# Kernel tuning notes

Measured on AMD Instinct MI355X. Metric: run time of the kernel, lower is better.

Reference implementation:

```python
import jax, jax.numpy as jnp
import numpy as np

DIM, D_STATE, D_CONV, EXPAND = 384, 16, 4, 2
D_INNER = EXPAND * DIM          # 768
DT_RANK = -(-DIM // 16)         # 24
B_, T_, H_, W_ = 2, 8, 16, 16
EPS = 1e-5


def layernorm(x, w, b):
    mu = x.mean(-1, keepdims=True)
    var = ((x - mu) ** 2).mean(-1, keepdims=True)
    return (x - mu) * jax.lax.rsqrt(var + EPS) * w + b


def setup_inputs() -> dict:
    key = jax.random.key(0)
    ks = jax.random.split(key, 12)
    std = 0.02
    x = jax.random.normal(ks[0], (B_, DIM, T_, H_, W_), jnp.float32)
    params = dict(
        ln1_w=jnp.ones((DIM,), jnp.float32),
        ln1_b=jnp.zeros((DIM,), jnp.float32),
        ln2_w=jnp.ones((DIM,), jnp.float32),
        ln2_b=jnp.zeros((DIM,), jnp.float32),
        in_proj_w=std * jax.random.normal(ks[1], (2 * D_INNER, DIM), jnp.float32),
        conv_w=std * jax.random.normal(ks[2], (D_INNER, 1, D_CONV), jnp.float32),
        conv_b=jnp.zeros((D_INNER,), jnp.float32),
        x_proj_w=std * jax.random.normal(ks[3], (DT_RANK + 2 * D_STATE, D_INNER), jnp.float32),
        dt_proj_w=std * jax.random.normal(ks[4], (D_INNER, DT_RANK), jnp.float32),
        dt_proj_b=0.01 * jax.random.normal(ks[5], (D_INNER,), jnp.float32),
        A_log=jnp.log(jnp.broadcast_to(jnp.arange(1, D_STATE + 1, dtype=jnp.float32), (D_INNER, D_STATE))),
        D=jnp.ones((D_INNER,), jnp.float32),
        out_proj_w=std * jax.random.normal(ks[6], (DIM, D_INNER), jnp.float32),
    )
    return {"x": x, **params}


def mamba(xn, in_proj_w, conv_w, conv_b, x_proj_w, dt_proj_w, dt_proj_b, A_log, D, out_proj_w):
    # xn: [B, L, dim]
    B, L, _ = xn.shape
    xz = xn @ in_proj_w.T                      # [B, L, 2*d_inner]
    u, z = jnp.split(xz, 2, axis=-1)
    # causal depthwise conv over tokens
    uc = jnp.transpose(u, (0, 2, 1))           # [B, d_inner, L]
    uc = jax.lax.conv_general_dilated(
        uc, conv_w, window_strides=(1,), padding=[(D_CONV - 1, 0)],
        dimension_numbers=("NCH", "OIH", "NCH"), feature_group_count=D_INNER)
    u = jax.nn.silu(jnp.transpose(uc, (0, 2, 1)) + conv_b)  # [B, L, d_inner]

    dbc = u @ x_proj_w.T                       # [B, L, dt_rank + 2*d_state]
    dt = dbc[..., :DT_RANK]
    Bm = dbc[..., DT_RANK:DT_RANK + D_STATE]   # [B, L, d_state]
    Cm = dbc[..., DT_RANK + D_STATE:]          # [B, L, d_state]
    delta = jax.nn.softplus(dt @ dt_proj_w.T + dt_proj_b)   # [B, L, d_inner]

    A = -jnp.exp(A_log)                        # [d_inner, d_state]
    deltaA = jnp.exp(delta[..., None] * A)                     # [B, L, d_inner, d_state]
    deltaBu = delta[..., None] * Bm[:, :, None, :] * u[..., None]

    def step(h, inp):
        dA, dBu, c = inp                       # [B,d_inner,d_state], [B,d_inner,d_state], [B,d_state]
        h = dA * h + dBu
        y = jnp.einsum("bds,bs->bd", h, c)
        return h, y

    h0 = jnp.zeros((B, D_INNER, D_STATE), xn.dtype)
    xs = (jnp.moveaxis(deltaA, 1, 0), jnp.moveaxis(deltaBu, 1, 0), jnp.moveaxis(Cm, 1, 0))
    _, ys = jax.lax.scan(step, h0, xs)
    y = jnp.moveaxis(ys, 0, 1)                 # [B, L, d_inner]
    y = y + u * D
    y = y * jax.nn.silu(z)
    return y @ out_proj_w.T                    # [B, L, dim]


def reference(x, ln1_w, ln1_b, ln2_w, ln2_b, in_proj_w, conv_w, conv_b,
              x_proj_w, dt_proj_w, dt_proj_b, A_log, D, out_proj_w):
    B, C, T, H, W = x.shape
    L = T * H * W
    x_flat = jnp.transpose(x.reshape(B, C, L), (0, 2, 1))   # [B, L, C]
    x_norm = layernorm(x_flat, ln1_w, ln1_b)
    x_mamba = mamba(x_norm, in_proj_w, conv_w, conv_b, x_proj_w,
                    dt_proj_w, dt_proj_b, A_log, D, out_proj_w)
    x_out = layernorm(x_flat + x_mamba, ln2_w, ln2_b)
    return jnp.transpose(x_out, (0, 2, 1)).reshape(B, C, T, H, W)
```

## Files before the change

kernel.cpp:

```cpp
#include <hip/hip_runtime.h>
#include <hip/hip_bf16.h>

typedef unsigned short u16;
typedef unsigned int   u32;
typedef __attribute__((ext_vector_type(8))) short short8;
typedef __attribute__((ext_vector_type(4))) float f32x4;

#define B_   2
#define L_   2048
#define CDIM 384
#define DI   768
#define DXZ  1536
#define DTR  24
#define DS   16
#define NDBC 56
#define NC   64
#define TC   32
#define TL   32
#define EPSV 1e-5f

#define OFFW_WIN  0
#define OFFW_WXP  589824
#define OFFW_WOUT 632832
#define TOTW      927744

__device__ __forceinline__ float bf2f(u16 u) {
    union { u32 i; float f; } v; v.i = ((u32)u) << 16; return v.f;
}
__device__ __forceinline__ u16 f2bf(float f) {
    union { float f; u32 i; } v; v.f = f;
    u32 x = v.i;
    u32 r = (x + 0x7FFFu + ((x >> 16) & 1u)) >> 16;
    return (u16)r;
}

__global__ __launch_bounds__(256) void ln1_convert(const float* __restrict__ x,
                                                   const float* __restrict__ w,
                                                   const float* __restrict__ bb,
                                                   u16* __restrict__ xn,
                                                   const float* __restrict__ win,
                                                   const float* __restrict__ wxp,
                                                   const float* __restrict__ wout,
                                                   u16* __restrict__ wdst) {
    __shared__ float tile[CDIM][TL + 1];
    __shared__ float red_s[8][TL];
    __shared__ float red_s2[8][TL];
    __shared__ float mu_s[TL], rs_s[TL];
    int tid = threadIdx.x, blk = blockIdx.x;
    if (blk >= 128) {
        int base = (blk - 128) * 256 + tid;
        for (int e = base; e < TOTW; e += 128 * 256) {
            float v;
            if (e < OFFW_WXP)       v = win[e];
            else if (e < OFFW_WOUT) v = wxp[e - OFFW_WXP];
            else                    v = wout[e - OFFW_WOUT];
            wdst[e] = f2bf(v);
        }
        return;
    }
    int b = blk >> 6;
    int l0 = (blk & 63) * TL;
    int cg = tid >> 5, li = tid & 31;
    const float* xp = x + (size_t)b * CDIM * L_ + l0 + li;
    float s = 0.f, s2 = 0.f;
#pragma unroll
    for (int c = cg; c < CDIM; c += 8) {
        float v = xp[(size_t)c * L_];
        tile[c][li] = v;
        s += v; s2 += v * v;
    }
    red_s[cg][li] = s; red_s2[cg][li] = s2;
    __syncthreads();
    if (tid < TL) {
        float ts = 0.f, ts2 = 0.f;
#pragma unroll
        for (int g = 0; g < 8; g++) { ts += red_s[g][tid]; ts2 += red_s2[g][tid]; }
        float mu = ts / CDIM;
        float var = ts2 / CDIM - mu * mu;
        mu_s[tid] = mu; rs_s[tid] = rsqrtf(var + EPSV);
    }
    __syncthreads();
    int wv = tid >> 6, lane = tid & 63;
#pragma unroll
    for (int r = 0; r < 8; r++) {
        int l = wv * 8 + r;
        float mu = mu_s[l], rs = rs_s[l];
        u16* op = xn + (size_t)(b * L_ + l0 + l) * CDIM;
#pragma unroll
        for (int j = 0; j < 6; j++) {
            int c = lane + 64 * j;
            float t = (tile[c][l] - mu) * rs * w[c] + bb[c];
            op[c] = f2bf(t);
        }
    }
}

template<int KN>
__global__ __launch_bounds__(256) void gemm_in(const u16* __restrict__ A,
                                               const u16* __restrict__ Bm,
                                               u16* __restrict__ Cp, int Nn) {
    int wave = threadIdx.x >> 6, lane = threadIdx.x & 63;
    int wm = wave & 1, wn = wave >> 1;
    int m0 = (blockIdx.x * 2 + wm) * 64;
    int n0 = (blockIdx.y * 2 + wn) * 64;
    int r = lane & 15, q = lane >> 4;
    f32x4 acc[4][4];
#pragma unroll
    for (int i = 0; i < 4; i++)
#pragma unroll
        for (int j = 0; j < 4; j++)
#pragma unroll
            for (int g = 0; g < 4; g++) acc[i][j][g] = 0.f;
#pragma unroll
    for (int k0 = 0; k0 < KN; k0 += 32) {
        short8 af[4], bf[4];
        int ka = k0 + q * 8;
#pragma unroll
        for (int i = 0; i < 4; i++) {
            af[i] = *(const short8*)(A + (size_t)(m0 + i * 16 + r) * KN + ka);
            bf[i] = *(const short8*)(Bm + (size_t)(n0 + i * 16 + r) * KN + ka);
        }
#pragma unroll
        for (int i = 0; i < 4; i++)
#pragma unroll
            for (int j = 0; j < 4; j++)
                acc[i][j] = __builtin_amdgcn_mfma_f32_16x16x32_bf16(af[i], bf[j], acc[i][j], 0, 0, 0);
    }
#pragma unroll
    for (int i = 0; i < 4; i++)
#pragma unroll
        for (int j = 0; j < 4; j++) {
            int col = n0 + j * 16 + r;
#pragma unroll
            for (int g = 0; g < 4; g++)
                Cp[(size_t)(m0 + i * 16 + q * 4 + g) * Nn + col] = f2bf(acc[i][j][g]);
        }
}

template<int KN, int NN>
__global__ __launch_bounds__(64) void gemm_out(const u16* __restrict__ A,
                                               const u16* __restrict__ Bm,
                                               float* __restrict__ Cp) {
    int lane = threadIdx.x;
    int m0 = blockIdx.x * 64, n0 = blockIdx.y * 64;
    int r = lane & 15, q = lane >> 4;
    f32x4 acc[4][4];
#pragma unroll
    for (int i = 0; i < 4; i++)
#pragma unroll
        for (int j = 0; j < 4; j++)
#pragma unroll
            for (int g = 0; g < 4; g++) acc[i][j][g] = 0.f;
#pragma unroll
    for (int k0 = 0; k0 < KN; k0 += 32) {
        short8 af[4], bf[4];
        int ka = k0 + q * 8;
#pragma unroll
        for (int i = 0; i < 4; i++) {
            af[i] = *(const short8*)(A + (size_t)(m0 + i * 16 + r) * KN + ka);
            bf[i] = *(const short8*)(Bm + (size_t)(n0 + i * 16 + r) * KN + ka);
        }
#pragma unroll
        for (int i = 0; i < 4; i++)
#pragma unroll
            for (int j = 0; j < 4; j++)
                acc[i][j] = __builtin_amdgcn_mfma_f32_16x16x32_bf16(af[i], bf[j], acc[i][j], 0, 0, 0);
    }
#pragma unroll
    for (int i = 0; i < 4; i++)
#pragma unroll
        for (int j = 0; j < 4; j++) {
            int col = n0 + j * 16 + r;
#pragma unroll
            for (int g = 0; g < 4; g++)
                Cp[(size_t)(m0 + i * 16 + q * 4 + g) * NN + col] = acc[i][j][g];
        }
}

template<int KN>
__global__ __launch_bounds__(64) void gemm_xp(const u16* __restrict__ A,
                                              const u16* __restrict__ Bm,
                                              float* __restrict__ Cp) {
    int lane = threadIdx.x;
    int m0 = blockIdx.x * 16;
    int r = lane & 15, q = lane >> 4;
    f32x4 acc[4];
#pragma unroll
    for (int j = 0; j < 4; j++)
#pragma unroll
        for (int g = 0; g < 4; g++) acc[j][g] = 0.f;
    short8 zf;
#pragma unroll
    for (int e = 0; e < 8; e++) zf[e] = 0;
#pragma unroll
    for (int k0 = 0; k0 < KN; k0 += 32) {
        int ka = k0 + q * 8;
        short8 af = *(const short8*)(A + (size_t)(m0 + r) * KN + ka);
        short8 bf[4];
#pragma unroll
        for (int j = 0; j < 4; j++) {
            int n = j * 16 + r;
            bf[j] = (n < NDBC) ? *(const short8*)(Bm + (size_t)n * KN + ka) : zf;
        }
#pragma unroll
        for (int j = 0; j < 4; j++)
            acc[j] = __builtin_amdgcn_mfma_f32_16x16x32_bf16(af, bf[j], acc[j], 0, 0, 0);
    }
#pragma unroll
    for (int j = 0; j < 4; j++) {
        int col = j * 16 + r;
        if (col < NDBC) {
#pragma unroll
            for (int g = 0; g < 4; g++)
                Cp[(size_t)(m0 + q * 4 + g) * NDBC + col] = acc[j][g];
        }
    }
}

__global__ __launch_bounds__(256) void conv_silu(const u16* __restrict__ xz,
                                                 const float* __restrict__ cw,
                                                 const float* __restrict__ cb,
                                                 u16* __restrict__ ubf) {
    int d = blockIdx.y * 256 + threadIdx.x;
    int m0 = blockIdx.x * 16;
    int l0 = m0 & (L_ - 1);
    float4 c4 = ((const float4*)cw)[d];
    float bias = cb[d];
    float w0, w1, w2;
    if (l0 == 0) { w0 = w1 = w2 = 0.f; }
    else {
        w0 = bf2f(xz[(size_t)(m0 - 3) * DXZ + d]);
        w1 = bf2f(xz[(size_t)(m0 - 2) * DXZ + d]);
        w2 = bf2f(xz[(size_t)(m0 - 1) * DXZ + d]);
    }
#pragma unroll
    for (int i = 0; i < 16; i++) {
        int m = m0 + i;
        float cur = bf2f(xz[(size_t)m * DXZ + d]);
        float acc = bias + w0 * c4.x + w1 * c4.y + w2 * c4.z + cur * c4.w;
        float sg = 1.f / (1.f + __expf(-acc));
        ubf[(size_t)m * DI + d] = f2bf(acc * sg);
        w0 = w1; w1 = w2; w2 = cur;
    }
}

__global__ __launch_bounds__(256) void scan_pass1(const u16* __restrict__ ubf,
                                                  const float* __restrict__ dbc,
                                                  const float* __restrict__ alogf,
                                                  const float* __restrict__ wdtf,
                                                  const float* __restrict__ bdtf,
                                                  float* __restrict__ chA,
                                                  float* __restrict__ chB) {
    int bc = blockIdx.x;
    int b = bc >> 6, chunk = bc & 63;
    int d = blockIdx.y * 256 + threadIdx.x;
    float a[DS], ap[DS], bv[DS], wdt[DTR];
#pragma unroll
    for (int s = 0; s < DS; s++) { a[s] = -__expf(alogf[d * DS + s]); ap[s] = 1.f; bv[s] = 0.f; }
#pragma unroll
    for (int k = 0; k < DTR; k++) wdt[k] = wdtf[d * DTR + k];
    float bd = bdtf[d];
    int t0 = b * L_ + chunk * TC;
#pragma unroll 2
    for (int t = t0; t < t0 + TC; t++) {
        const float* row = dbc + (size_t)t * NDBC;
        float acc = bd;
#pragma unroll
        for (int k = 0; k < DTR; k++) acc += row[k] * wdt[k];
        float dd = (acc > 20.f) ? acc : __logf(1.f + __expf(acc));
        float du = dd * bf2f(ubf[(size_t)t * DI + d]);
#pragma unroll
        for (int s = 0; s < DS; s++) {
            float dA = __expf(dd * a[s]);
            bv[s] = dA * bv[s] + du * row[DTR + s];
            ap[s] *= dA;
        }
    }
    float* pa = chA + ((size_t)bc * DI + d) * DS;
    float* pb = chB + ((size_t)bc * DI + d) * DS;
#pragma unroll
    for (int s = 0; s < DS; s++) { pa[s] = ap[s]; pb[s] = bv[s]; }
}

__global__ __launch_bounds__(256) void scan_mid(const float* __restrict__ chA,
                                                const float* __restrict__ chB,
                                                float* __restrict__ hin) {
    int idx = blockIdx.x * 256 + threadIdx.x;
    int b = idx / (DI * DS);
    int rem = idx - b * (DI * DS);
    float h = 0.f;
#pragma unroll 4
    for (int c = 0; c < NC; c++) {
        size_t off = ((size_t)(b * NC + c) * DI) * DS + rem;
        hin[off] = h;
        h = chA[off] * h + chB[off];
    }
}

__global__ __launch_bounds__(256) void scan_pass2(const u16* __restrict__ ubf,
                                                  const float* __restrict__ dbc,
                                                  const float* __restrict__ alogf,
                                                  const float* __restrict__ wdtf,
                                                  const float* __restrict__ bdtf,
                                                  const float* __restrict__ hin,
                                                  const float* __restrict__ Dwf,
                                                  const u16* __restrict__ xz,
                                                  u16* __restrict__ ym) {
    int bc = blockIdx.x;
    int b = bc >> 6, chunk = bc & 63;
    int d = blockIdx.y * 256 + threadIdx.x;
    float a[DS], h[DS], wdt[DTR];
#pragma unroll
    for (int s = 0; s < DS; s++) a[s] = -__expf(alogf[d * DS + s]);
#pragma unroll
    for (int k = 0; k < DTR; k++) wdt[k] = wdtf[d * DTR + k];
    float bd = bdtf[d];
    const float* hp = hin + ((size_t)bc * DI + d) * DS;
    float h0[DS];
#pragma unroll
    for (int s = 0; s < DS; s++) h[s] = hp[s];
    float dD = Dwf[d];
    int t0 = b * L_ + chunk * TC;
#pragma unroll 2
    for (int t = t0; t < t0 + TC; t++) {
        const float* row = dbc + (size_t)t * NDBC;
        float acc = bd;
#pragma unroll
        for (int k = 0; k < DTR; k++) acc += row[k] * wdt[k];
        float dd = (acc > 20.f) ? acc : __logf(1.f + __expf(acc));
        float uu = bf2f(ubf[(size_t)t * DI + d]);
        float du = dd * uu;
        float y = 0.f;
#pragma unroll
        for (int s = 0; s < DS; s++) {
            float dA = __expf(dd * a[s]);
            h[s] = dA * h[s] + du * row[DTR + s];
            y += h[s] * row[DTR + DS + s];
        }
        float z = bf2f(xz[(size_t)t * DXZ + DI + d]);
        float sg = 1.f / (1.f + __expf(-z));
        ym[(size_t)t * DI + d] = f2bf((y + uu * dD) * (z * sg));
    }
}

__global__ __launch_bounds__(256) void ln2_out(const float* __restrict__ x,
                                               const float* __restrict__ om,
                                               const float* __restrict__ w,
                                               const float* __restrict__ bb,
                                               float* __restrict__ out) {
    __shared__ float tile[CDIM][TL + 1];
    __shared__ float mu_s[TL], rs_s[TL];
    int tid = threadIdx.x, blk = blockIdx.x;
    int b = blk >> 6;
    int l0 = (blk & 63) * TL;
    int cg = tid >> 5, li = tid & 31;
    const float* xp = x + (size_t)b * CDIM * L_ + l0 + li;
#pragma unroll
    for (int c = cg; c < CDIM; c += 8) tile[c][li] = xp[(size_t)c * L_];
    __syncthreads();
    int wv = tid >> 6, lane = tid & 63;
#pragma unroll
    for (int r = 0; r < 8; r++) {
        int l = wv * 8 + r;
        const float* op = om + (size_t)(b * L_ + l0 + l) * CDIM;
        float s = 0.f, s2 = 0.f;
#pragma unroll
        for (int j = 0; j < 6; j++) {
            int c = lane + 64 * j;
            float t = tile[c][l] + op[c];
            tile[c][l] = t;
            s += t; s2 += t * t;
        }
#pragma unroll
        for (int off = 32; off > 0; off >>= 1) { s += __shfl_xor(s, off); s2 += __shfl_xor(s2, off); }
        if (lane == 0) {
            float mu = s / CDIM;
            float var = s2 / CDIM - mu * mu;
            mu_s[l] = mu; rs_s[l] = rsqrtf(var + EPSV);
        }
    }
    __syncthreads();
    float* outp = out + (size_t)b * CDIM * L_ + l0 + li;
    float mu = mu_s[li], rs = rs_s[li];
#pragma unroll
    for (int c = cg; c < CDIM; c += 8) {
        float t = (tile[c][li] - mu) * rs * w[c] + bb[c];
        outp[(size_t)c * L_] = t;
    }
}

extern "C" void kernel_launch(void* const* d_in, const int* in_sizes, int n_in,
                              void* d_out, int out_size, void* d_ws, size_t ws_size,
                              hipStream_t stream) {
    const float* x    = (const float*)d_in[0];
    const float* ln1w = (const float*)d_in[1];
    const float* ln1b = (const float*)d_in[2];
    const float* ln2w = (const float*)d_in[3];
    const float* ln2b = (const float*)d_in[4];
    const float* win  = (const float*)d_in[5];
    const float* cw   = (const float*)d_in[6];
    const float* cb   = (const float*)d_in[7];
    const float* wxp  = (const float*)d_in[8];
    const float* wdt  = (const float*)d_in[9];
    const float* bdt  = (const float*)d_in[10];
    const float* alog = (const float*)d_in[11];
    const float* Dw   = (const float*)d_in[12];
    const float* wout = (const float*)d_in[13];

    char* ws = (char*)d_ws;
    u16*   wbf   = (u16*)(ws + 0);
    u16*   win_b  = wbf + OFFW_WIN;
    u16*   wxp_b  = wbf + OFFW_WXP;
    u16*   wout_b = wbf + OFFW_WOUT;
    u16*   xn    = (u16*)(ws + 1855488);
    u16*   xz    = (u16*)(ws + 5001216);
    u16*   ubf   = (u16*)(ws + 17584128);
    float* dbc   = (float*)(ws + 23875584);
    float* chA   = (float*)(ws + 24793088);
    float* chB   = (float*)(ws + 31084544);
    float* hin   = (float*)(ws + 37376000);
    u16*   ym    = (u16*)(ws + 43667456);
    float* om    = (float*)(ws + 49958912);

    ln1_convert<<<dim3(256), 256, 0, stream>>>(x, ln1w, ln1b, xn, win, wxp, wout, wbf);
    gemm_in<384><<<dim3(32, 12), 256, 0, stream>>>(xn, win_b, xz, DXZ);
    conv_silu<<<dim3(256, 3), 256, 0, stream>>>(xz, cw, cb, ubf);
    gemm_xp<768><<<dim3(256), 64, 0, stream>>>(ubf, wxp_b, dbc);
    scan_pass1<<<dim3(128, 3), 256, 0, stream>>>(ubf, dbc, alog, wdt, bdt, chA, chB);
    scan_mid<<<96, 256, 0, stream>>>(chA, chB, hin);
    scan_pass2<<<dim3(128, 3), 256, 0, stream>>>(ubf, dbc, alog, wdt, bdt, hin, Dw, xz, ym);
    gemm_out<768, 384><<<dim3(64, 6), 64, 0, stream>>>(ym, wout_b, om);
    ln2_out<<<dim3(128), 256, 0, stream>>>(x, om, ln2w, ln2b, (float*)d_out);
}
```

Measured before the change: 223.0 us.

## Split-K across four waves in out/x projections; transpose chunk-state layout

The output and x-projection GEMMs now run four waves per block. Each wave handles a quarter of K, and the partial tiles are reduced through shared memory, so each tile has four times as many waves to hide latency. The chunk state arrays chA/chB/hin are re-laid out with d_inner as the fastest dimension, which makes the scan_pass1 writes and scan_pass2 reads coalesced across threads. The cost is two block barriers plus shared-memory traffic for the reduction. The layout must also stay consistent with scan_mid, which indexes by a flat offset and so remains correct.

```diff
diff --git a/kernel.cpp b/kernel.cpp
--- a/kernel.cpp
+++ b/kernel.cpp
@@ -138,10 +138,11 @@
 }
 
 template<int KN, int NN>
-__global__ __launch_bounds__(64) void gemm_out(const u16* __restrict__ A,
-                                               const u16* __restrict__ Bm,
-                                               float* __restrict__ Cp) {
-    int lane = threadIdx.x;
+__global__ __launch_bounds__(256) void gemm_out(const u16* __restrict__ A,
+                                                const u16* __restrict__ Bm,
+                                                float* __restrict__ Cp) {
+    __shared__ float sm[2][64][66];
+    int lane = threadIdx.x & 63, wave = threadIdx.x >> 6;
     int m0 = blockIdx.x * 64, n0 = blockIdx.y * 64;
     int r = lane & 15, q = lane >> 4;
     f32x4 acc[4][4];
@@ -151,10 +152,12 @@
         for (int j = 0; j < 4; j++)
 #pragma unroll
             for (int g = 0; g < 4; g++) acc[i][j][g] = 0.f;
-#pragma unroll
-    for (int k0 = 0; k0 < KN; k0 += 32) {
+    const int KQ = KN / 4;
+    int kb = wave * KQ;
+#pragma unroll
+    for (int k0 = 0; k0 < KQ; k0 += 32) {
         short8 af[4], bf[4];
-        int ka = k0 + q * 8;
+        int ka = kb + k0 + q * 8;
 #pragma unroll
         for (int i = 0; i < 4; i++) {
             af[i] = *(const short8*)(A + (size_t)(m0 + i * 16 + r) * KN + ka);
@@ -166,22 +169,39 @@
             for (int j = 0; j < 4; j++)
                 acc[i][j] = __builtin_amdgcn_mfma_f32_16x16x32_bf16(af[i], bf[j], acc[i][j], 0, 0, 0);
     }
-#pragma unroll
-    for (int i = 0; i < 4; i++)
-#pragma unroll
-        for (int j = 0; j < 4; j++) {
-            int col = n0 + j * 16 + r;
-#pragma unroll
-            for (int g = 0; g < 4; g++)
-                Cp[(size_t)(m0 + i * 16 + q * 4 + g) * NN + col] = acc[i][j][g];
-        }
+    if (wave < 2) {
+#pragma unroll
+        for (int i = 0; i < 4; i++)
+#pragma unroll
+            for (int j = 0; j < 4; j++)
+#pragma unroll
+                for (int g = 0; g < 4; g++)
+                    sm[wave][i * 16 + q * 4 + g][j * 16 + r] = acc[i][j][g];
+    }
+    __syncthreads();
+    if (wave >= 2) {
+        int w2 = wave - 2;
+#pragma unroll
+        for (int i = 0; i < 4; i++)
+#pragma unroll
+            for (int j = 0; j < 4; j++)
+#pragma unroll
+                for (int g = 0; g < 4; g++)
+                    sm[w2][i * 16 + q * 4 + g][j * 16 + r] += acc[i][j][g];
+    }
+    __syncthreads();
+    for (int e = threadIdx.x; e < 64 * 64; e += 256) {
+        int row = e >> 6, col = e & 63;
+        Cp[(size_t)(m0 + row) * NN + n0 + col] = sm[0][row][col] + sm[1][row][col];
+    }
 }
 
 template<int KN>
-__global__ __launch_bounds__(64) void gemm_xp(const u16* __restrict__ A,
-                                              const u16* __restrict__ Bm,
-                                              float* __restrict__ Cp) {
-    int lane = threadIdx.x;
+__global__ __launch_bounds__(256) void gemm_xp(const u16* __restrict__ A,
+                                               const u16* __restrict__ Bm,
+                                               float* __restrict__ Cp) {
+    __shared__ float sm[2][16][66];
+    int lane = threadIdx.x & 63, wave = threadIdx.x >> 6;
     int m0 = blockIdx.x * 16;
     int r = lane & 15, q = lane >> 4;
     f32x4 acc[4];
@@ -192,9 +212,11 @@
     short8 zf;
 #pragma unroll
     for (int e = 0; e < 8; e++) zf[e] = 0;
-#pragma unroll
-    for (int k0 = 0; k0 < KN; k0 += 32) {
-        int ka = k0 + q * 8;
+    const int KQ = KN / 4;
+    int kb = wave * KQ;
+#pragma unroll
+    for (int k0 = 0; k0 < KQ; k0 += 32) {
+        int ka = kb + k0 + q * 8;
         short8 af = *(const short8*)(A + (size_t)(m0 + r) * KN + ka);
         short8 bf[4];
 #pragma unroll
@@ -206,13 +228,27 @@
         for (int j = 0; j < 4; j++)
             acc[j] = __builtin_amdgcn_mfma_f32_16x16x32_bf16(af, bf[j], acc[j], 0, 0, 0);
     }
-#pragma unroll
-    for (int j = 0; j < 4; j++) {
-        int col = j * 16 + r;
+    if (wave < 2) {
+#pragma unroll
+        for (int j = 0; j < 4; j++)
+#pragma unroll
+            for (int g = 0; g < 4; g++)
+                sm[wave][q * 4 + g][j * 16 + r] = acc[j][g];
+    }
+    __syncthreads();
+    if (wave >= 2) {
+        int w2 = wave - 2;
+#pragma unroll
+        for (int j = 0; j < 4; j++)
+#pragma unroll
+            for (int g = 0; g < 4; g++)
+                sm[w2][q * 4 + g][j * 16 + r] += acc[j][g];
+    }
+    __syncthreads();
+    for (int e = threadIdx.x; e < 16 * 64; e += 256) {
+        int row = e >> 6, col = e & 63;
         if (col < NDBC) {
-#pragma unroll
-            for (int g = 0; g < 4; g++)
-                Cp[(size_t)(m0 + q * 4 + g) * NDBC + col] = acc[j][g];
+            Cp[(size_t)(m0 + row) * NDBC + col] = sm[0][row][col] + sm[1][row][col];
         }
     }
 }
@@ -276,10 +312,10 @@
             ap[s] *= dA;
         }
     }
-    float* pa = chA + ((size_t)bc * DI + d) * DS;
-    float* pb = chB + ((size_t)bc * DI + d) * DS;
-#pragma unroll
-    for (int s = 0; s < DS; s++) { pa[s] = ap[s]; pb[s] = bv[s]; }
+    float* pa = chA + (size_t)bc * DS * DI + d;
+    float* pb = chB + (size_t)bc * DS * DI + d;
+#pragma unroll
+    for (int s = 0; s < DS; s++) { pa[(size_t)s * DI] = ap[s]; pb[(size_t)s * DI] = bv[s]; }
 }
 
 __global__ __launch_bounds__(256) void scan_mid(const float* __restrict__ chA,
@@ -315,10 +351,9 @@
 #pragma unroll
     for (int k = 0; k < DTR; k++) wdt[k] = wdtf[d * DTR + k];
     float bd = bdtf[d];
-    const float* hp = hin + ((size_t)bc * DI + d) * DS;
-    float h0[DS];
-#pragma unroll
-    for (int s = 0; s < DS; s++) h[s] = hp[s];
+    const float* hp = hin + (size_t)bc * DS * DI + d;
+#pragma unroll
+    for (int s = 0; s < DS; s++) h[s] = hp[(size_t)s * DI];
     float dD = Dwf[d];
     int t0 = b * L_ + chunk * TC;
 #pragma unroll 2
@@ -425,10 +460,10 @@
     ln1_convert<<<dim3(256), 256, 0, stream>>>(x, ln1w, ln1b, xn, win, wxp, wout, wbf);
     gemm_in<384><<<dim3(32, 12), 256, 0, stream>>>(xn, win_b, xz, DXZ);
     conv_silu<<<dim3(256, 3), 256, 0, stream>>>(xz, cw, cb, ubf);
-    gemm_xp<768><<<dim3(256), 64, 0, stream>>>(ubf, wxp_b, dbc);
+    gemm_xp<768><<<dim3(256), 256, 0, stream>>>(ubf, wxp_b, dbc);
     scan_pass1<<<dim3(128, 3), 256, 0, stream>>>(ubf, dbc, alog, wdt, bdt, chA, chB);
     scan_mid<<<96, 256, 0, stream>>>(chA, chB, hin);
     scan_pass2<<<dim3(128, 3), 256, 0, stream>>>(ubf, dbc, alog, wdt, bdt, hin, Dw, xz, ym);
-    gemm_out<768, 384><<<dim3(64, 6), 64, 0, stream>>>(ym, wout_b, om);
+    gemm_out<768, 384><<<dim3(64, 6), 256, 0, stream>>>(ym, wout_b, om);
     ln2_out<<<dim3(128), 256, 0, stream>>>(x, om, ln2w, ln2b, (float*)d_out);
 }
```

Result: no change. 219.7 us (-1.5%).

## Fuse x_proj GEMM into scan pass 1 and out_proj GEMM into scan pass 2

Applied to the files above, without the earlier changes.

The x_proj GEMM now runs inside the first scan kernel, split over K across 12 waves and reduced through shared memory. The resulting dbc chunk is kept in LDS for the scan and still written to global memory for pass 2. The second scan pass writes its gated output into a swizzled LDS tile and runs the out_proj MFMA GEMM in place, so the ym intermediate and two kernel launches disappear. The chunk-state buffers also switch to a state-major layout so global stores and loads are coalesced across d. In exchange, the scan kernels now launch only 128 blocks of 768 threads, which uses fewer CUs and puts more pressure on registers and LDS.

```diff
diff --git a/kernel.cpp b/kernel.cpp
--- a/kernel.cpp
+++ b/kernel.cpp
@@ -137,86 +137,6 @@
         }
 }
 
-template<int KN, int NN>
-__global__ __launch_bounds__(64) void gemm_out(const u16* __restrict__ A,
-                                               const u16* __restrict__ Bm,
-                                               float* __restrict__ Cp) {
-    int lane = threadIdx.x;
-    int m0 = blockIdx.x * 64, n0 = blockIdx.y * 64;
-    int r = lane & 15, q = lane >> 4;
-    f32x4 acc[4][4];
-#pragma unroll
-    for (int i = 0; i < 4; i++)
-#pragma unroll
-        for (int j = 0; j < 4; j++)
-#pragma unroll
-            for (int g = 0; g < 4; g++) acc[i][j][g] = 0.f;
-#pragma unroll
-    for (int k0 = 0; k0 < KN; k0 += 32) {
-        short8 af[4], bf[4];
-        int ka = k0 + q * 8;
-#pragma unroll
-        for (int i = 0; i < 4; i++) {
-            af[i] = *(const short8*)(A + (size_t)(m0 + i * 16 + r) * KN + ka);
-            bf[i] = *(const short8*)(Bm + (size_t)(n0 + i * 16 + r) * KN + ka);
-        }
-#pragma unroll
-        for (int i = 0; i < 4; i++)
-#pragma unroll
-            for (int j = 0; j < 4; j++)
-                acc[i][j] = __builtin_amdgcn_mfma_f32_16x16x32_bf16(af[i], bf[j], acc[i][j], 0, 0, 0);
-    }
-#pragma unroll
-    for (int i = 0; i < 4; i++)
-#pragma unroll
-        for (int j = 0; j < 4; j++) {
-            int col = n0 + j * 16 + r;
-#pragma unroll
-            for (int g = 0; g < 4; g++)
-                Cp[(size_t)(m0 + i * 16 + q * 4 + g) * NN + col] = acc[i][j][g];
-        }
-}
-
-template<int KN>
-__global__ __launch_bounds__(64) void gemm_xp(const u16* __restrict__ A,
-                                              const u16* __restrict__ Bm,
-                                              float* __restrict__ Cp) {
-    int lane = threadIdx.x;
-    int m0 = blockIdx.x * 16;
-    int r = lane & 15, q = lane >> 4;
-    f32x4 acc[4];
-#pragma unroll
-    for (int j = 0; j < 4; j++)
-#pragma unroll
-        for (int g = 0; g < 4; g++) acc[j][g] = 0.f;
-    short8 zf;
-#pragma unroll
-    for (int e = 0; e < 8; e++) zf[e] = 0;
-#pragma unroll
-    for (int k0 = 0; k0 < KN; k0 += 32) {
-        int ka = k0 + q * 8;
-        short8 af = *(const short8*)(A + (size_t)(m0 + r) * KN + ka);
-        short8 bf[4];
-#pragma unroll
-        for (int j = 0; j < 4; j++) {
-            int n = j * 16 + r;
-            bf[j] = (n < NDBC) ? *(const short8*)(Bm + (size_t)n * KN + ka) : zf;
-        }
-#pragma unroll
-        for (int j = 0; j < 4; j++)
-            acc[j] = __builtin_amdgcn_mfma_f32_16x16x32_bf16(af, bf[j], acc[j], 0, 0, 0);
-    }
-#pragma unroll
-    for (int j = 0; j < 4; j++) {
-        int col = j * 16 + r;
-        if (col < NDBC) {
-#pragma unroll
-            for (int g = 0; g < 4; g++)
-                Cp[(size_t)(m0 + q * 4 + g) * NDBC + col] = acc[j][g];
-        }
-    }
-}
-
 __global__ __launch_bounds__(256) void conv_silu(const u16* __restrict__ xz,
                                                  const float* __restrict__ cw,
                                                  const float* __restrict__ cb,
@@ -244,42 +164,90 @@
     }
 }
 
-__global__ __launch_bounds__(256) void scan_pass1(const u16* __restrict__ ubf,
-                                                  const float* __restrict__ dbc,
-                                                  const float* __restrict__ alogf,
-                                                  const float* __restrict__ wdtf,
-                                                  const float* __restrict__ bdtf,
-                                                  float* __restrict__ chA,
-                                                  float* __restrict__ chB) {
+__global__ __launch_bounds__(768) void xp_scan1(const u16* __restrict__ ubf,
+                                                const u16* __restrict__ wxpb,
+                                                const float* __restrict__ alogf,
+                                                const float* __restrict__ wdtf,
+                                                const float* __restrict__ bdtf,
+                                                float* __restrict__ dbc,
+                                                float* __restrict__ chA,
+                                                float* __restrict__ chB) {
+    __shared__ float smR[12][16][68];
+    __shared__ float dbcS[TC][NDBC + 1];
+    int tid = threadIdx.x;
     int bc = blockIdx.x;
-    int b = bc >> 6, chunk = bc & 63;
-    int d = blockIdx.y * 256 + threadIdx.x;
-    float a[DS], ap[DS], bv[DS], wdt[DTR];
-#pragma unroll
-    for (int s = 0; s < DS; s++) { a[s] = -__expf(alogf[d * DS + s]); ap[s] = 1.f; bv[s] = 0.f; }
-#pragma unroll
-    for (int k = 0; k < DTR; k++) wdt[k] = wdtf[d * DTR + k];
-    float bd = bdtf[d];
-    int t0 = b * L_ + chunk * TC;
+    int t0g = (bc >> 6) * L_ + (bc & 63) * TC;
+    {
+        int wave = tid >> 6, lane = tid & 63;
+        int mi = wave & 1, ks = wave >> 1;
+        int r = lane & 15, q = lane >> 4;
+        f32x4 acc[4];
+#pragma unroll
+        for (int j = 0; j < 4; j++)
+#pragma unroll
+            for (int g = 0; g < 4; g++) acc[j][g] = 0.f;
+        short8 zf;
+#pragma unroll
+        for (int e = 0; e < 8; e++) zf[e] = 0;
+        int kb = ks * 128;
+#pragma unroll
+        for (int k0 = 0; k0 < 128; k0 += 32) {
+            int ka = kb + k0 + q * 8;
+            short8 af = *(const short8*)(ubf + (size_t)(t0g + mi * 16 + r) * DI + ka);
+            short8 bfv[4];
+#pragma unroll
+            for (int j = 0; j < 4; j++) {
+                int n = j * 16 + r;
+                bfv[j] = (n < NDBC) ? *(const short8*)(wxpb + (size_t)n * DI + ka) : zf;
+            }
+#pragma unroll
+            for (int j = 0; j < 4; j++)
+                acc[j] = __builtin_amdgcn_mfma_f32_16x16x32_bf16(af, bfv[j], acc[j], 0, 0, 0);
+        }
+#pragma unroll
+        for (int j = 0; j < 4; j++)
+#pragma unroll
+            for (int g = 0; g < 4; g++)
+                smR[wave][q * 4 + g][j * 16 + r] = acc[j][g];
+    }
+    __syncthreads();
+    for (int e = tid; e < TC * NDBC; e += 768) {
+        int row = e / NDBC, col = e - row * NDBC;
+        int mi = row >> 4, rr = row & 15;
+        float v = 0.f;
+#pragma unroll
+        for (int ks = 0; ks < 6; ks++) v += smR[ks * 2 + mi][rr][col];
+        dbcS[row][col] = v;
+        dbc[(size_t)(t0g + row) * NDBC + col] = v;
+    }
+    __syncthreads();
+    {
+        int d = tid;
+        float a[DS], ap[DS], bv[DS], wdtv[DTR];
+#pragma unroll
+        for (int s = 0; s < DS; s++) { a[s] = -__expf(alogf[d * DS + s]); ap[s] = 1.f; bv[s] = 0.f; }
+#pragma unroll
+        for (int k = 0; k < DTR; k++) wdtv[k] = wdtf[d * DTR + k];
+        float bd = bdtf[d];
 #pragma unroll 2
-    for (int t = t0; t < t0 + TC; t++) {
-        const float* row = dbc + (size_t)t * NDBC;
-        float acc = bd;
-#pragma unroll
-        for (int k = 0; k < DTR; k++) acc += row[k] * wdt[k];
-        float dd = (acc > 20.f) ? acc : __logf(1.f + __expf(acc));
-        float du = dd * bf2f(ubf[(size_t)t * DI + d]);
-#pragma unroll
-        for (int s = 0; s < DS; s++) {
-            float dA = __expf(dd * a[s]);
-            bv[s] = dA * bv[s] + du * row[DTR + s];
-            ap[s] *= dA;
-        }
-    }
-    float* pa = chA + ((size_t)bc * DI + d) * DS;
-    float* pb = chB + ((size_t)bc * DI + d) * DS;
-#pragma unroll
-    for (int s = 0; s < DS; s++) { pa[s] = ap[s]; pb[s] = bv[s]; }
+        for (int t = 0; t < TC; t++) {
+            float acc = bd;
+#pragma unroll
+            for (int k = 0; k < DTR; k++) acc += dbcS[t][k] * wdtv[k];
+            float dd = (acc > 20.f) ? acc : __logf(1.f + __expf(acc));
+            float du = dd * bf2f(ubf[(size_t)(t0g + t) * DI + d]);
+#pragma unroll
+            for (int s = 0; s < DS; s++) {
+                float dA = __expf(dd * a[s]);
+                bv[s] = dA * bv[s] + du * dbcS[t][DTR + s];
+                ap[s] *= dA;
+            }
+        }
+        float* pa = chA + (size_t)bc * DS * DI + d;
+        float* pb = chB + (size_t)bc * DS * DI + d;
+#pragma unroll
+        for (int s = 0; s < DS; s++) { pa[(size_t)s * DI] = ap[s]; pb[(size_t)s * DI] = bv[s]; }
+    }
 }
 
 __global__ __launch_bounds__(256) void scan_mid(const float* __restrict__ chA,
@@ -297,49 +265,90 @@
     }
 }
 
-__global__ __launch_bounds__(256) void scan_pass2(const u16* __restrict__ ubf,
-                                                  const float* __restrict__ dbc,
-                                                  const float* __restrict__ alogf,
-                                                  const float* __restrict__ wdtf,
-                                                  const float* __restrict__ bdtf,
-                                                  const float* __restrict__ hin,
-                                                  const float* __restrict__ Dwf,
-                                                  const u16* __restrict__ xz,
-                                                  u16* __restrict__ ym) {
+__global__ __launch_bounds__(768) void scan2_outproj(const u16* __restrict__ ubf,
+                                                     const float* __restrict__ dbc,
+                                                     const float* __restrict__ alogf,
+                                                     const float* __restrict__ wdtf,
+                                                     const float* __restrict__ bdtf,
+                                                     const float* __restrict__ hin,
+                                                     const float* __restrict__ Dwf,
+                                                     const u16* __restrict__ xz,
+                                                     const u16* __restrict__ woutb,
+                                                     float* __restrict__ om) {
+    __shared__ float dbcS[TC][NDBC + 1];
+    __shared__ __align__(16) u16 ymS[TC * DI];
+    int tid = threadIdx.x;
     int bc = blockIdx.x;
-    int b = bc >> 6, chunk = bc & 63;
-    int d = blockIdx.y * 256 + threadIdx.x;
-    float a[DS], h[DS], wdt[DTR];
-#pragma unroll
-    for (int s = 0; s < DS; s++) a[s] = -__expf(alogf[d * DS + s]);
-#pragma unroll
-    for (int k = 0; k < DTR; k++) wdt[k] = wdtf[d * DTR + k];
-    float bd = bdtf[d];
-    const float* hp = hin + ((size_t)bc * DI + d) * DS;
-    float h0[DS];
-#pragma unroll
-    for (int s = 0; s < DS; s++) h[s] = hp[s];
-    float dD = Dwf[d];
-    int t0 = b * L_ + chunk * TC;
+    int t0g = (bc >> 6) * L_ + (bc & 63) * TC;
+    for (int e = tid; e < TC * NDBC; e += 768) {
+        int row = e / NDBC, col = e - row * NDBC;
+        dbcS[row][col] = dbc[(size_t)(t0g + row) * NDBC + col];
+    }
+    __syncthreads();
+    {
+        int d = tid;
+        float a[DS], h[DS], wdtv[DTR];
+#pragma unroll
+        for (int s = 0; s < DS; s++) a[s] = -__expf(alogf[d * DS + s]);
+#pragma unroll
+        for (int k = 0; k < DTR; k++) wdtv[k] = wdtf[d * DTR + k];
+        float bd = bdtf[d];
+        const float* hp = hin + (size_t)bc * DS * DI + d;
+#pragma unroll
+        for (int s = 0; s < DS; s++) h[s] = hp[(size_t)s * DI];
+        float dD = Dwf[d];
 #pragma unroll 2
-    for (int t = t0; t < t0 + TC; t++) {
-        const float* row = dbc + (size_t)t * NDBC;
-        float acc = bd;
-#pragma unroll
-        for (int k = 0; k < DTR; k++) acc += row[k] * wdt[k];
-        float dd = (acc > 20.f) ? acc : __logf(1.f + __expf(acc));
-        float uu = bf2f(ubf[(size_t)t * DI + d]);
-        float du = dd * uu;
-        float y = 0.f;
-#pragma unroll
-        for (int s = 0; s < DS; s++) {
-            float dA = __expf(dd * a[s]);
-            h[s] = dA * h[s] + du * row[DTR + s];
-            y += h[s] * row[DTR + DS + s];
-        }
-        float z = bf2f(xz[(size_t)t * DXZ + DI + d]);
-        float sg = 1.f / (1.f + __expf(-z));
-        ym[(size_t)t * DI + d] = f2bf((y + uu * dD) * (z * sg));
+        for (int t = 0; t < TC; t++) {
+            float acc = bd;
+#pragma unroll
+            for (int k = 0; k < DTR; k++) acc += dbcS[t][k] * wdtv[k];
+            float dd = (acc > 20.f) ? acc : __logf(1.f + __expf(acc));
+            float uu = bf2f(ubf[(size_t)(t0g + t) * DI + d]);
+            float du = dd * uu;
+            float y = 0.f;
+#pragma unroll
+            for (int s = 0; s < DS; s++) {
+                float dA = __expf(dd * a[s]);
+                h[s] = dA * h[s] + du * dbcS[t][DTR + s];
+                y += h[s] * dbcS[t][DTR + DS + s];
+            }
+            float z = bf2f(xz[(size_t)(t0g + t) * DXZ + DI + d]);
+            float sg = 1.f / (1.f + __expf(-z));
+            ymS[t * DI + (d ^ ((t & 7) << 3))] = f2bf((y + uu * dD) * (z * sg));
+        }
+    }
+    __syncthreads();
+    {
+        int wave = tid >> 6, lane = tid & 63;
+        int mi = wave & 1, ni = wave >> 1;
+        int r = lane & 15, q = lane >> 4;
+        int n0 = ni * 64;
+        f32x4 acc[4];
+#pragma unroll
+        for (int j = 0; j < 4; j++)
+#pragma unroll
+            for (int g = 0; g < 4; g++) acc[j][g] = 0.f;
+        int tl = mi * 16 + r;
+        int xw = (tl & 7) << 3;
+#pragma unroll
+        for (int k0 = 0; k0 < DI; k0 += 32) {
+            int ka = k0 + q * 8;
+            short8 af = *(const short8*)(&ymS[tl * DI + (ka ^ xw)]);
+            short8 bfv[4];
+#pragma unroll
+            for (int j = 0; j < 4; j++)
+                bfv[j] = *(const short8*)(woutb + (size_t)(n0 + j * 16 + r) * DI + ka);
+#pragma unroll
+            for (int j = 0; j < 4; j++)
+                acc[j] = __builtin_amdgcn_mfma_f32_16x16x32_bf16(af, bfv[j], acc[j], 0, 0, 0);
+        }
+#pragma unroll
+        for (int j = 0; j < 4; j++) {
+            int col = n0 + j * 16 + r;
+#pragma unroll
+            for (int g = 0; g < 4; g++)
+                om[(size_t)(t0g + mi * 16 + q * 4 + g) * CDIM + col] = acc[j][g];
+        }
     }
 }
 
@@ -419,16 +428,13 @@
     float* chA   = (float*)(ws + 24793088);
     float* chB   = (float*)(ws + 31084544);
     float* hin   = (float*)(ws + 37376000);
-    u16*   ym    = (u16*)(ws + 43667456);
     float* om    = (float*)(ws + 49958912);
 
     ln1_convert<<<dim3(256), 256, 0, stream>>>(x, ln1w, ln1b, xn, win, wxp, wout, wbf);
     gemm_in<384><<<dim3(32, 12), 256, 0, stream>>>(xn, win_b, xz, DXZ);
     conv_silu<<<dim3(256, 3), 256, 0, stream>>>(xz, cw, cb, ubf);
-    gemm_xp<768><<<dim3(256), 64, 0, stream>>>(ubf, wxp_b, dbc);
-    scan_pass1<<<dim3(128, 3), 256, 0, stream>>>(ubf, dbc, alog, wdt, bdt, chA, chB);
+    xp_scan1<<<dim3(128), 768, 0, stream>>>(ubf, wxp_b, alog, wdt, bdt, dbc, chA, chB);
     scan_mid<<<96, 256, 0, stream>>>(chA, chB, hin);
-    scan_pass2<<<dim3(128, 3), 256, 0, stream>>>(ubf, dbc, alog, wdt, bdt, hin, Dw, xz, ym);
-    gemm_out<768, 384><<<dim3(64, 6), 64, 0, stream>>>(ym, wout_b, om);
+    scan2_outproj<<<dim3(128), 768, 0, stream>>>(ubf, dbc, alog, wdt, bdt, hin, Dw, xz, wout_b, om);
     ln2_out<<<dim3(128), 256, 0, stream>>>(x, om, ln2w, ln2b, (float*)d_out);
 }
```

Result: slower. 260.0 us (+16.6%).
